# Kernel optimization log

Measured on AMD Instinct MI355X. Metric: run time of the kernel, lower is better.

Reference implementation:

```python
import jax, jax.numpy as jnp
import numpy as np
from jax import lax

# Izhikevich parameters (buffers in the torch module, constants here)
A, B_P, C_P, D_P, DT = 0.02, 0.2, -65.0, 6.0, 0.2
V_INIT = -65.0
V_THRESH = 30.0


def setup_inputs() -> dict:
    key = jax.random.key(0)
    I_seq = jax.random.normal(key, (16, 1000, 4096), dtype=jnp.float32)  # [B, T, D]
    return {"I_seq": I_seq}


def reference(I_seq) -> jnp.ndarray:
    B, T, D = I_seq.shape
    # torch flattens [B,T,D] -> [B*D, T]; we scan over time so use [T, B*D]
    I_t = jnp.transpose(I_seq, (1, 0, 2)).reshape(T, B * D)
    v0 = jnp.full((B * D,), V_INIT, dtype=I_seq.dtype)
    u0 = B_P * v0

    def step(carry, i_t):
        v, u = carry
        dv = 0.04 * v * v + 5.0 * v + 140.0 - u + i_t
        v = v + DT * dv
        du = A * (B_P * v - u)
        u = u + DT * du
        spk = (v >= V_THRESH).astype(v.dtype)
        v = jnp.where(spk > 0.0, C_P, v)
        u = jnp.where(spk > 0.0, u + D_P, u)
        return (v, u), spk

    (_, _), spikes = lax.scan(step, (v0, u0), I_t)  # spikes: [T, B*D]
    spikes = spikes.reshape(T, B, D).transpose(1, 0, 2)  # [B, T, D]
    return spikes
```

## Files before the change

kernel.cpp:

```cpp
#include <hip/hip_runtime.h>


constexpr int T_STEPS = 1000;
constexpr int D_DIM   = 4096;
constexpr int U       = 25;
constexpr int NB      = T_STEPS / U;

__global__ __launch_bounds__(256, 1)
void izhikevich_kernel(const float* __restrict__ I, float* __restrict__ out, int BD) {
    #pragma clang fp contract(off)
    int n = blockIdx.x * 256 + threadIdx.x;
    if (n >= BD) return;
    int b = n / D_DIM;
    int d = n % D_DIM;
    const size_t base = (size_t)b * T_STEPS * D_DIM + d;
    const float* ip = I + base;
    float*       op = out + base;

    float v = -65.0f;
    float u = 0.2f * -65.0f;

    auto step = [&](float i_t, float* o) {
        float dv = 0.04f * v * v + 5.0f * v + 140.0f - u + i_t;
        v = v + 0.2f * dv;
        float du = 0.02f * (0.2f * v - u);
        u = u + 0.2f * du;
        bool s = (v >= 30.0f);
        __builtin_nontemporal_store(s ? 1.0f : 0.0f, o);
        if (s) { v = -65.0f; u = u + 6.0f; }
    };

    float buf[4][U];

    #pragma unroll
    for (int j = 0; j < U; ++j)
        buf[0][j] = __builtin_nontemporal_load(ip + (size_t)j * D_DIM);
    #pragma unroll
    for (int j = 0; j < U; ++j)
        buf[1][j] = __builtin_nontemporal_load(ip + (size_t)(U + j) * D_DIM);

    for (int ob = 0; ob < NB; ob += 4) {
        #pragma unroll
        for (int p = 0; p < 4; ++p) {
            int bb = ob + p;
            if (bb + 2 < NB) {
                const float* pp = ip + (size_t)(bb + 2) * U * D_DIM;
                #pragma unroll
                for (int j = 0; j < U; ++j)
                    buf[(p + 2) & 3][j] =
                        __builtin_nontemporal_load(pp + (size_t)j * D_DIM);
            }
            float* oo = op + (size_t)bb * U * D_DIM;
            #pragma unroll
            for (int j = 0; j < U; ++j)
                step(buf[p][j], oo + (size_t)j * D_DIM);
        }
    }
}

extern "C" void kernel_launch(void* const* d_in, const int* in_sizes, int n_in,
                              void* d_out, int out_size, void* d_ws, size_t ws_size,
                              hipStream_t stream) {
    const float* I  = (const float*)d_in[0];
    float*      out = (float*)d_out;
    int total = in_sizes[0];
    int BD    = total / T_STEPS;
    int block = 256;
    int grid  = (BD + block - 1) / block;
    izhikevich_kernel<<<grid, block, 0, stream>>>(I, out, BD);
}
```

Measured before the change: 418.4 us.

## Process four neurons per thread with float4 loads and stores

Each thread now advances four adjacent neurons using 16-byte vector loads and nontemporal stores, with 64-thread blocks and a shorter prefetch block of 10 timesteps. This aims to cut memory instruction count and add instruction-level parallelism across the four independent recurrences. In exchange, the total wave count drops fourfold to one wave per CU, and the prefetched bytes in flight shrink, which may expose memory latency.

```diff
diff --git a/kernel.cpp b/kernel.cpp
--- a/kernel.cpp
+++ b/kernel.cpp
@@ -3,57 +3,68 @@
 
 constexpr int T_STEPS = 1000;
 constexpr int D_DIM   = 4096;
-constexpr int U       = 25;
+constexpr int U       = 10;
 constexpr int NB      = T_STEPS / U;
 
-__global__ __launch_bounds__(256, 1)
-void izhikevich_kernel(const float* __restrict__ I, float* __restrict__ out, int BD) {
+typedef float v4f __attribute__((ext_vector_type(4)));
+
+__global__ __launch_bounds__(64, 1)
+void izhikevich_kernel(const float* __restrict__ I, float* __restrict__ out, int NQ) {
     #pragma clang fp contract(off)
-    int n = blockIdx.x * 256 + threadIdx.x;
-    if (n >= BD) return;
-    int b = n / D_DIM;
-    int d = n % D_DIM;
+    int n = blockIdx.x * 64 + threadIdx.x;
+    if (n >= NQ) return;
+    int e0 = n * 4;
+    int b = e0 / D_DIM;
+    int d = e0 % D_DIM;
     const size_t base = (size_t)b * T_STEPS * D_DIM + d;
-    const float* ip = I + base;
-    float*       op = out + base;
+    const v4f* ip = (const v4f*)(I + base);
+    v4f*       op = (v4f*)(out + base);
+    constexpr size_t STRIDE = D_DIM / 4;
 
-    float v = -65.0f;
-    float u = 0.2f * -65.0f;
+    float v[4], u[4];
+    #pragma unroll
+    for (int k = 0; k < 4; ++k) { v[k] = -65.0f; u[k] = 0.2f * -65.0f; }
 
-    auto step = [&](float i_t, float* o) {
-        float dv = 0.04f * v * v + 5.0f * v + 140.0f - u + i_t;
-        v = v + 0.2f * dv;
-        float du = 0.02f * (0.2f * v - u);
-        u = u + 0.2f * du;
-        bool s = (v >= 30.0f);
-        __builtin_nontemporal_store(s ? 1.0f : 0.0f, o);
-        if (s) { v = -65.0f; u = u + 6.0f; }
-    };
-
-    float buf[4][U];
+    v4f buf[4][U];
 
     #pragma unroll
     for (int j = 0; j < U; ++j)
-        buf[0][j] = __builtin_nontemporal_load(ip + (size_t)j * D_DIM);
+        buf[0][j] = __builtin_nontemporal_load(ip + (size_t)j * STRIDE);
     #pragma unroll
     for (int j = 0; j < U; ++j)
-        buf[1][j] = __builtin_nontemporal_load(ip + (size_t)(U + j) * D_DIM);
+        buf[1][j] = __builtin_nontemporal_load(ip + (size_t)(U + j) * STRIDE);
+
+    auto step = [&](v4f iv, v4f* o) {
+        v4f ov;
+        #pragma unroll
+        for (int k = 0; k < 4; ++k) {
+            float i_t = iv[k];
+            float dv = 0.04f * v[k] * v[k] + 5.0f * v[k] + 140.0f - u[k] + i_t;
+            v[k] = v[k] + 0.2f * dv;
+            float du = 0.02f * (0.2f * v[k] - u[k]);
+            u[k] = u[k] + 0.2f * du;
+            bool s = (v[k] >= 30.0f);
+            ov[k] = s ? 1.0f : 0.0f;
+            if (s) { v[k] = -65.0f; u[k] = u[k] + 6.0f; }
+        }
+        __builtin_nontemporal_store(ov, o);
+    };
 
     for (int ob = 0; ob < NB; ob += 4) {
         #pragma unroll
         for (int p = 0; p < 4; ++p) {
             int bb = ob + p;
             if (bb + 2 < NB) {
-                const float* pp = ip + (size_t)(bb + 2) * U * D_DIM;
+                const v4f* pp = ip + (size_t)(bb + 2) * U * STRIDE;
                 #pragma unroll
                 for (int j = 0; j < U; ++j)
                     buf[(p + 2) & 3][j] =
-                        __builtin_nontemporal_load(pp + (size_t)j * D_DIM);
+                        __builtin_nontemporal_load(pp + (size_t)j * STRIDE);
             }
-            float* oo = op + (size_t)bb * U * D_DIM;
+            v4f* oo = op + (size_t)bb * U * STRIDE;
             #pragma unroll
             for (int j = 0; j < U; ++j)
-                step(buf[p][j], oo + (size_t)j * D_DIM);
+                step(buf[p][j], oo + (size_t)j * STRIDE);
         }
     }
 }
@@ -65,7 +76,8 @@
     float*      out = (float*)d_out;
     int total = in_sizes[0];
     int BD    = total / T_STEPS;
-    int block = 256;
-    int grid  = (BD + block - 1) / block;
-    izhikevich_kernel<<<grid, block, 0, stream>>>(I, out, BD);
+    int NQ    = BD / 4;
+    int block = 64;
+    int grid  = (NQ + block - 1) / block;
+    izhikevich_kernel<<<grid, block, 0, stream>>>(I, out, NQ);
 }
```

New measurement: 453.5 us. +8.4%, slower.
